# Kernel optimization log

Hardware: AMD Instinct MI355X
Metric: run time of the kernel (lower is better)

The kernel has to match this reference:

```python
import jax, jax.numpy as jnp
from jax import lax
import numpy as np

T, N, C, D, K = 256, 4096, 12, 256, 12


def setup_inputs() -> dict:
    key = jax.random.key(0)
    ks = jax.random.split(key, 11)
    g = lambda k, shape: (jax.random.normal(k, shape, jnp.float32) * 0.05)
    return {
        "x": jax.random.normal(ks[0], (T, N, C), jnp.float32),
        "enc_Wx": g(ks[1], (D, C)),
        "enc_bx": g(ks[2], (D,)),
        "enc_Wh": g(ks[3], (D, D)),
        "enc_Wy": g(ks[4], (K, D)),
        "enc_by": g(ks[5], (K,)),
        "dec_Wx": g(ks[6], (D, C)),
        "dec_bx": g(ks[7], (D,)),
        "dec_Wh": g(ks[8], (D, D)),
        "dec_Wy": g(ks[9], (K, D)),
        "dec_by": g(ks[10], (K,)),
    }


def reference(x, enc_Wx, enc_bx, enc_Wh, enc_Wy, enc_by,
              dec_Wx, dec_bx, dec_Wh, dec_Wy, dec_by):
    # x: (T, N, C)
    Tn, Nn, Cn = x.shape
    Dn = enc_Wh.shape[0]

    # ---- encoder Elman RNN: h_t = relu(x2h(x_t) + h2h(h_{t-1})) ----
    # Precompute input projection for all timesteps (batched GEMM),
    # leaving only the D x D recurrence inside the scan.
    x_proj = jnp.einsum('tnc,dc->tnd', x, enc_Wx) + enc_bx  # (T, N, D)

    def enc_step(h, xp):
        h = jax.nn.relu(xp + h @ enc_Wh.T)
        return h, None

    h0 = jnp.zeros((Nn, Dn), x.dtype)
    h_last, _ = lax.scan(enc_step, h0, x_proj)  # (N, D) == enc_h[-1]
    # (encoder h2y output is computed in the original but discarded)

    # ---- decoder: greedy feedback loop, T steps ----
    sos0 = jnp.zeros((Nn, Cn), x.dtype).at[:, -2].set(1.0)

    def dec_step(carry, _):
        h, sos = carry
        h = jax.nn.relu(sos @ dec_Wx.T + dec_bx + h @ dec_Wh.T)  # (N, D)
        y = h @ dec_Wy.T + dec_by                                # (N, K)
        sos = jax.nn.one_hot(jnp.argmax(y, axis=-1), y.shape[-1],
                             dtype=x.dtype)                      # (N, C)
        return (h, sos), y

    _, ys = lax.scan(dec_step, (h_last, sos0), None, length=Tn)
    return ys  # (T, N, K)
```

## Files before the change

### kernel.cpp

```cpp
#include <hip/hip_runtime.h>
#include <cstdint>
#include <cstddef>

#define TT 256
#define NN 4096
#define CC 12
#define DD 256
#define KD 12
#define NB 16
#define NTH 512
#define HS 264
#define XS 40
#define YS 20

typedef _Float16 half8 __attribute__((ext_vector_type(8)));
typedef float f32x4 __attribute__((ext_vector_type(4)));
#define MFMA __builtin_amdgcn_mfma_f32_16x16x32_f16

struct FalseC { static constexpr bool value = false; };
struct TrueC  { static constexpr bool value = true;  };

struct alignas(16) SM {
  _Float16 hhi[2][NB][HS];
  _Float16 hlo[2][NB][HS];
  _Float16 xhi[4][NB][XS];
  _Float16 xlo[4][NB][XS];
  float    part2[2][8][NB][YS];
};

__device__ __forceinline__ void split8(const float* w, half8& hi, half8& lo) {
  #pragma unroll
  for (int j = 0; j < 8; ++j) {
    _Float16 h = (_Float16)w[j];
    hi[j] = h;
    lo[j] = (_Float16)(w[j] - (float)h);
  }
}

__device__ __forceinline__ unsigned pack2(_Float16 a, _Float16 b) {
  union { _Float16 h[2]; unsigned u; } x;
  x.h[0] = a; x.h[1] = b;
  return x.u;
}

__device__ __forceinline__ void BAR() {
  asm volatile("s_waitcnt lgkmcnt(0)" ::: "memory");
  __builtin_amdgcn_s_barrier();
  __builtin_amdgcn_sched_barrier(0);
}

__global__ __launch_bounds__(NTH, 2)
void seq2seq_kernel(const float* __restrict__ x,
                    const float* __restrict__ enc_Wx,
                    const float* __restrict__ enc_bx,
                    const float* __restrict__ enc_Wh,
                    const float* __restrict__ dec_Wx,
                    const float* __restrict__ dec_bx,
                    const float* __restrict__ dec_Wh,
                    const float* __restrict__ dec_Wy,
                    const float* __restrict__ dec_by,
                    float* __restrict__ out)
{
  __shared__ SM sm;
  const int tid  = (int)threadIdx.x;
  const int wid  = tid >> 6;
  const int lane = tid & 63;
  const int l15  = lane & 15;
  const int quad = lane >> 4;
  const int n0   = (int)blockIdx.x * NB;

  half8 Whi[2][8], Wlo[2][8];
  half8 Xhi[2], Xlo[2];
  float bxr[2];
  float pfA0 = 0.f, pfA1 = 0.f, pfA2 = 0.f;
  float pfB0 = 0.f, pfB1 = 0.f, pfB2 = 0.f;

  if (wid == 1) {
    const float* xg = x + ((size_t)1 * NN + n0) * CC;
    pfB0 = xg[lane]; pfB1 = xg[lane + 64]; pfB2 = xg[lane + 128];
  }

  auto loadWh = [&](const float* __restrict__ W) {
    #pragma unroll
    for (int tt = 0; tt < 2; ++tt) {
      const int n = wid * 32 + 2 * l15 + tt;
      #pragma unroll
      for (int c = 0; c < 8; ++c) {
        float w[8];
        const float* p = W + (size_t)n * DD + c * 32 + quad * 8;
        *(float4*)&w[0] = *(const float4*)p;
        *(float4*)&w[4] = *(const float4*)(p + 4);
        split8(w, Whi[tt][c], Wlo[tt][c]);
      }
    }
  };
  auto loadWx = [&](const float* __restrict__ Wx) {
    #pragma unroll
    for (int tt = 0; tt < 2; ++tt) {
      const int n = wid * 32 + 2 * l15 + tt;
      float w[8];
      #pragma unroll
      for (int j = 0; j < 8; ++j) {
        const int k = quad * 8 + j;
        w[j] = (k < CC) ? Wx[(size_t)n * CC + k] : 0.f;
      }
      split8(w, Xhi[tt], Xlo[tt]);
    }
  };
  auto loadBx = [&](const float* __restrict__ bx) {
    #pragma unroll
    for (int tt = 0; tt < 2; ++tt) bxr[tt] = bx[wid * 32 + 2 * l15 + tt];
  };

  {
    unsigned* z;
    z = (unsigned*)&sm.hhi[0][0][0];
    for (int i = tid; i < NB * HS / 2; i += NTH) z[i] = 0u;
    z = (unsigned*)&sm.hlo[0][0][0];
    for (int i = tid; i < NB * HS / 2; i += NTH) z[i] = 0u;
    z = (unsigned*)&sm.xhi[0][0][0];
    for (int i = tid; i < 4 * NB * XS / 2; i += NTH) z[i] = 0u;
    z = (unsigned*)&sm.xlo[0][0][0];
    for (int i = tid; i < 4 * NB * XS / 2; i += NTH) z[i] = 0u;
  }
  loadWh(enc_Wh);
  loadWx(enc_Wx);
  loadBx(enc_bx);
  BAR();
  if (tid < NB * CC) {
    const float v = x[(size_t)n0 * CC + tid];
    const _Float16 h = (_Float16)v;
    sm.xhi[0][tid / CC][tid % CC] = h;
    sm.xlo[0][tid / CC][tid % CC] = (_Float16)(v - (float)h);
  }
  BAR();

  auto encStep = [&](int t, auto IAc) {
    constexpr bool IA = decltype(IAc)::value;
    if (wid == 1) {
      const int tp = (t + 2 < TT) ? (t + 2) : (TT - 1);
      const float* xg = x + ((size_t)tp * NN + n0) * CC;
      if constexpr (IA) { pfA0 = xg[lane]; pfA1 = xg[lane + 64]; pfA2 = xg[lane + 128]; }
      else              { pfB0 = xg[lane]; pfB1 = xg[lane + 64]; pfB2 = xg[lane + 128]; }
    }
    const int rb = t & 1, wb = rb ^ 1, xs = t & 3;
    f32x4 aA0 = {0.f,0.f,0.f,0.f}, aA1 = {0.f,0.f,0.f,0.f};
    f32x4 aB0 = {0.f,0.f,0.f,0.f}, aB1 = {0.f,0.f,0.f,0.f};
    const half8 xh = *(const half8*)&sm.xhi[xs][l15][quad * 8];
    const half8 xl = *(const half8*)&sm.xlo[xs][l15][quad * 8];
    aA0 = MFMA(xh, Xhi[0], aA0, 0, 0, 0);
    aA1 = MFMA(xh, Xhi[1], aA1, 0, 0, 0);
    aB0 = MFMA(xl, Xhi[0], aB0, 0, 0, 0);
    aB1 = MFMA(xl, Xhi[1], aB1, 0, 0, 0);
    aB0 = MFMA(xh, Xlo[0], aB0, 0, 0, 0);
    aB1 = MFMA(xh, Xlo[1], aB1, 0, 0, 0);
    const _Float16* hh = &sm.hhi[rb][l15][0];
    const _Float16* hl = &sm.hlo[rb][l15][0];
    #pragma unroll
    for (int c = 0; c < 8; ++c) {
      const half8 ahi = *(const half8*)(hh + c * 32 + quad * 8);
      const half8 alo = *(const half8*)(hl + c * 32 + quad * 8);
      aA0 = MFMA(ahi, Whi[0][c], aA0, 0, 0, 0);
      aA1 = MFMA(ahi, Whi[1][c], aA1, 0, 0, 0);
      aB0 = MFMA(alo, Whi[0][c], aB0, 0, 0, 0);
      aB1 = MFMA(alo, Whi[1][c], aB1, 0, 0, 0);
      aA0 = MFMA(ahi, Wlo[0][c], aA0, 0, 0, 0);
      aA1 = MFMA(ahi, Wlo[1][c], aA1, 0, 0, 0);
    }
    const int colh = wid * 32 + 2 * l15;
    #pragma unroll
    for (int r = 0; r < 4; ++r) {
      const int m = quad * 4 + r;
      const float v0 = fmaxf(aA0[r] + aB0[r] + bxr[0], 0.f);
      const float v1 = fmaxf(aA1[r] + aB1[r] + bxr[1], 0.f);
      const _Float16 h0 = (_Float16)v0, h1 = (_Float16)v1;
      *(unsigned*)&sm.hhi[wb][m][colh] = pack2(h0, h1);
      *(unsigned*)&sm.hlo[wb][m][colh] =
          pack2((_Float16)(v0 - (float)h0), (_Float16)(v1 - (float)h1));
    }
    if (wid == 1) {
      const int xw = (t + 1) & 3;
      float w0, w1, w2;
      if constexpr (IA) { w0 = pfB0; w1 = pfB1; w2 = pfB2; }
      else              { w0 = pfA0; w1 = pfA1; w2 = pfA2; }
      #pragma unroll
      for (int j = 0; j < 3; ++j) {
        const int i = lane + 64 * j;
        const float vv = (j == 0) ? w0 : (j == 1) ? w1 : w2;
        const _Float16 hx = (_Float16)vv;
        sm.xhi[xw][i / CC][i % CC] = hx;
        sm.xlo[xw][i / CC][i % CC] = (_Float16)(vv - (float)hx);
      }
    }
    BAR();
  };

  for (int t = 0; t < TT; t += 2) {
    encStep(t, TrueC{});
    encStep(t + 1, FalseC{});
  }

  loadWh(dec_Wh);
  loadWx(dec_Wx);
  loadBx(dec_bx);
  float by4[4];
  #pragma unroll
  for (int j = 0; j < 4; ++j) {
    const int o = quad * 4 + j;
    by4[j] = (o < KD) ? dec_by[o] : 0.f;
  }
  half8 wyh, wyl;
  {
    float w[8];
    if (l15 < KD) {
      const float* p = dec_Wy + (size_t)l15 * DD + wid * 32 + quad * 8;
      *(float4*)&w[0] = *(const float4*)p;
      *(float4*)&w[4] = *(const float4*)(p + 4);
    } else {
      #pragma unroll
      for (int j = 0; j < 8; ++j) w[j] = 0.f;
    }
    split8(w, wyh, wyl);
  }
  half8 aX;
  #pragma unroll
  for (int j = 0; j < 8; ++j)
    aX[j] = (_Float16)((quad * 8 + j == CC - 2) ? 1.f : 0.f);
  BAR();

  for (int t = 0; t < TT; ++t) {
    const int rb = t & 1, wb = rb ^ 1, pb = t & 1;
    f32x4 aA0 = {0.f,0.f,0.f,0.f}, aA1 = {0.f,0.f,0.f,0.f};
    f32x4 aB0 = {0.f,0.f,0.f,0.f}, aB1 = {0.f,0.f,0.f,0.f};
    aA0 = MFMA(aX, Xhi[0], aA0, 0, 0, 0);
    aA1 = MFMA(aX, Xhi[1], aA1, 0, 0, 0);
    aB0 = MFMA(aX, Xlo[0], aB0, 0, 0, 0);
    aB1 = MFMA(aX, Xlo[1], aB1, 0, 0, 0);
    const _Float16* hh = &sm.hhi[rb][l15][0];
    const _Float16* hl = &sm.hlo[rb][l15][0];
    #pragma unroll
    for (int c = 0; c < 8; ++c) {
      const half8 ahi = *(const half8*)(hh + c * 32 + quad * 8);
      const half8 alo = *(const half8*)(hl + c * 32 + quad * 8);
      aA0 = MFMA(ahi, Whi[0][c], aA0, 0, 0, 0);
      aA1 = MFMA(ahi, Whi[1][c], aA1, 0, 0, 0);
      aB0 = MFMA(alo, Whi[0][c], aB0, 0, 0, 0);
      aB1 = MFMA(alo, Whi[1][c], aB1, 0, 0, 0);
      aA0 = MFMA(ahi, Wlo[0][c], aA0, 0, 0, 0);
      aA1 = MFMA(ahi, Wlo[1][c], aA1, 0, 0, 0);
    }
    const int colh = wid * 32 + 2 * l15;
    #pragma unroll
    for (int r = 0; r < 4; ++r) {
      const int m = quad * 4 + r;
      const float v0 = fmaxf(aA0[r] + aB0[r] + bxr[0], 0.f);
      const float v1 = fmaxf(aA1[r] + aB1[r] + bxr[1], 0.f);
      const _Float16 h0 = (_Float16)v0, h1 = (_Float16)v1;
      *(unsigned*)&sm.hhi[wb][m][colh] = pack2(h0, h1);
      *(unsigned*)&sm.hlo[wb][m][colh] =
          pack2((_Float16)(v0 - (float)h0), (_Float16)(v1 - (float)h1));
    }
    asm volatile("s_waitcnt lgkmcnt(0)" ::: "memory");
    const half8 yh8 = *(const half8*)&sm.hhi[wb][l15][wid * 32 + quad * 8];
    const half8 yl8 = *(const half8*)&sm.hlo[wb][l15][wid * 32 + quad * 8];
    f32x4 yp = {0.f,0.f,0.f,0.f};
    yp = MFMA(yh8, wyh, yp, 0, 0, 0);
    yp = MFMA(yl8, wyh, yp, 0, 0, 0);
    yp = MFMA(yh8, wyl, yp, 0, 0, 0);
    #pragma unroll
    for (int r = 0; r < 4; ++r)
      sm.part2[pb][wid][quad * 4 + r][l15] = yp[r];
    BAR();
    f32x4 ys = *(const f32x4*)&sm.part2[pb][0][l15][quad * 4];
    #pragma unroll
    for (int w = 1; w < 8; ++w)
      ys += *(const f32x4*)&sm.part2[pb][w][l15][quad * 4];
    float yv[4];
    #pragma unroll
    for (int j = 0; j < 4; ++j) yv[j] = ys[j] + by4[j];
    if (wid == 0 && quad < 3) {
      float4 st; st.x = yv[0]; st.y = yv[1]; st.z = yv[2]; st.w = yv[3];
      *(float4*)&out[((size_t)t * NN + n0 + l15) * KD + quad * 4] = st;
    }
    float v = -1e30f; int io = 0;
    #pragma unroll
    for (int j = 0; j < 4; ++j) {
      const int o = quad * 4 + j;
      const float cv = (o < KD) ? yv[j] : -1e30f;
      const bool take = cv > v;
      io = take ? o : io;
      v  = take ? cv : v;
    }
    #pragma unroll
    for (int d = 16; d < 64; d <<= 1) {
      const float ov = __shfl_xor(v, d);
      const int   oi = __shfl_xor(io, d);
      const bool take = (ov > v) || (ov == v && oi < io);
      v  = take ? ov : v;
      io = take ? oi : io;
    }
    #pragma unroll
    for (int j = 0; j < 8; ++j)
      aX[j] = (_Float16)((quad * 8 + j == io) ? 1.f : 0.f);
  }
}

extern "C" void kernel_launch(void* const* d_in, const int* in_sizes, int n_in,
                              void* d_out, int out_size, void* d_ws, size_t ws_size,
                              hipStream_t stream) {
  (void)in_sizes; (void)n_in; (void)d_ws; (void)ws_size; (void)out_size;
  const float* x      = (const float*)d_in[0];
  const float* enc_Wx = (const float*)d_in[1];
  const float* enc_bx = (const float*)d_in[2];
  const float* enc_Wh = (const float*)d_in[3];
  const float* dec_Wx = (const float*)d_in[6];
  const float* dec_bx = (const float*)d_in[7];
  const float* dec_Wh = (const float*)d_in[8];
  const float* dec_Wy = (const float*)d_in[9];
  const float* dec_by = (const float*)d_in[10];
  float* outp = (float*)d_out;

  seq2seq_kernel<<<NN / NB, NTH, 0, stream>>>(
      x, enc_Wx, enc_bx, enc_Wh, dec_Wx, dec_bx, dec_Wh, dec_Wy, dec_by, outp);
}
```

Measured before the change: 820.5 us.

## Software-pipeline encoder input projection one step ahead and use packed fp16 conversion

The encoder now computes the input-projection MFMAs for step t+1 after the recurrent MFMAs of step t, keeping them in a second set of accumulators. This moves the x-projection and its LDS reads off the critical path that follows each barrier. The x prefetch distance grows by one step and two x slots are preloaded at start. Hidden-state hi/lo splitting now uses the packed round-toward-zero conversion (cvt_pkrtz) instead of separate scalar conversions, which changes rounding of the hi part, and the extra accumulators raise register pressure.

New measurement: 798.0 us. 2.7% less time.

```diff
diff --git a/kernel.cpp b/kernel.cpp
--- a/kernel.cpp
+++ b/kernel.cpp
@@ -14,6 +14,7 @@
 #define YS 20
 
 typedef _Float16 half8 __attribute__((ext_vector_type(8)));
+typedef __fp16 fp16x2 __attribute__((ext_vector_type(2)));
 typedef float f32x4 __attribute__((ext_vector_type(4)));
 #define MFMA __builtin_amdgcn_mfma_f32_16x16x32_f16
 
@@ -37,10 +38,13 @@
   }
 }
 
-__device__ __forceinline__ unsigned pack2(_Float16 a, _Float16 b) {
-  union { _Float16 h[2]; unsigned u; } x;
-  x.h[0] = a; x.h[1] = b;
-  return x.u;
+__device__ __forceinline__ void packpair(float v0, float v1,
+                                         unsigned& hw, unsigned& lw) {
+  union { fp16x2 v; unsigned u; } a, b;
+  a.v = __builtin_amdgcn_cvt_pkrtz(v0, v1);
+  const float r0 = (float)a.v[0], r1 = (float)a.v[1];
+  b.v = __builtin_amdgcn_cvt_pkrtz(v0 - r0, v1 - r1);
+  hw = a.u; lw = b.u;
 }
 
 __device__ __forceinline__ void BAR() {
@@ -74,11 +78,7 @@
   float bxr[2];
   float pfA0 = 0.f, pfA1 = 0.f, pfA2 = 0.f;
   float pfB0 = 0.f, pfB1 = 0.f, pfB2 = 0.f;
-
-  if (wid == 1) {
-    const float* xg = x + ((size_t)1 * NN + n0) * CC;
-    pfB0 = xg[lane]; pfB1 = xg[lane + 64]; pfB2 = xg[lane + 128];
-  }
+  f32x4 accP[4], accQ[4];
 
   auto loadWh = [&](const float* __restrict__ W) {
     #pragma unroll
@@ -126,67 +126,80 @@
   loadWh(enc_Wh);
   loadWx(enc_Wx);
   loadBx(enc_bx);
+  if (wid == 1) {
+    const float* xg = x + ((size_t)2 * NN + n0) * CC;
+    pfB0 = xg[lane]; pfB1 = xg[lane + 64]; pfB2 = xg[lane + 128];
+  }
   BAR();
-  if (tid < NB * CC) {
-    const float v = x[(size_t)n0 * CC + tid];
-    const _Float16 h = (_Float16)v;
-    sm.xhi[0][tid / CC][tid % CC] = h;
-    sm.xlo[0][tid / CC][tid % CC] = (_Float16)(v - (float)h);
+  #pragma unroll
+  for (int s = 0; s < 2; ++s) {
+    if (tid < NB * CC) {
+      const float v = x[((size_t)s * NN + n0) * CC + tid];
+      const _Float16 h = (_Float16)v;
+      sm.xhi[s][tid / CC][tid % CC] = h;
+      sm.xlo[s][tid / CC][tid % CC] = (_Float16)(v - (float)h);
+    }
   }
   BAR();
-
-  auto encStep = [&](int t, auto IAc) {
-    constexpr bool IA = decltype(IAc)::value;
-    if (wid == 1) {
-      const int tp = (t + 2 < TT) ? (t + 2) : (TT - 1);
-      const float* xg = x + ((size_t)tp * NN + n0) * CC;
-      if constexpr (IA) { pfA0 = xg[lane]; pfA1 = xg[lane + 64]; pfA2 = xg[lane + 128]; }
-      else              { pfB0 = xg[lane]; pfB1 = xg[lane + 64]; pfB2 = xg[lane + 128]; }
-    }
-    const int rb = t & 1, wb = rb ^ 1, xs = t & 3;
-    f32x4 aA0 = {0.f,0.f,0.f,0.f}, aA1 = {0.f,0.f,0.f,0.f};
-    f32x4 aB0 = {0.f,0.f,0.f,0.f}, aB1 = {0.f,0.f,0.f,0.f};
-    const half8 xh = *(const half8*)&sm.xhi[xs][l15][quad * 8];
-    const half8 xl = *(const half8*)&sm.xlo[xs][l15][quad * 8];
-    aA0 = MFMA(xh, Xhi[0], aA0, 0, 0, 0);
-    aA1 = MFMA(xh, Xhi[1], aA1, 0, 0, 0);
-    aB0 = MFMA(xl, Xhi[0], aB0, 0, 0, 0);
-    aB1 = MFMA(xl, Xhi[1], aB1, 0, 0, 0);
-    aB0 = MFMA(xh, Xlo[0], aB0, 0, 0, 0);
-    aB1 = MFMA(xh, Xlo[1], aB1, 0, 0, 0);
+  #pragma unroll
+  for (int i = 0; i < 4; ++i) accP[i] = (f32x4){0.f, 0.f, 0.f, 0.f};
+  {
+    const half8 xh = *(const half8*)&sm.xhi[0][l15][quad * 8];
+    const half8 xl = *(const half8*)&sm.xlo[0][l15][quad * 8];
+    accP[0] = MFMA(xh, Xhi[0], accP[0], 0, 0, 0);
+    accP[1] = MFMA(xh, Xhi[1], accP[1], 0, 0, 0);
+    accP[2] = MFMA(xl, Xhi[0], accP[2], 0, 0, 0);
+    accP[3] = MFMA(xl, Xhi[1], accP[3], 0, 0, 0);
+    accP[2] = MFMA(xh, Xlo[0], accP[2], 0, 0, 0);
+    accP[3] = MFMA(xh, Xlo[1], accP[3], 0, 0, 0);
+  }
+
+  auto encCore = [&](int t, f32x4 (&cur)[4], f32x4 (&nxt)[4],
+                     float pw0, float pw1, float pw2) {
+    const int rb = t & 1, wb = rb ^ 1;
     const _Float16* hh = &sm.hhi[rb][l15][0];
     const _Float16* hl = &sm.hlo[rb][l15][0];
     #pragma unroll
     for (int c = 0; c < 8; ++c) {
       const half8 ahi = *(const half8*)(hh + c * 32 + quad * 8);
       const half8 alo = *(const half8*)(hl + c * 32 + quad * 8);
-      aA0 = MFMA(ahi, Whi[0][c], aA0, 0, 0, 0);
-      aA1 = MFMA(ahi, Whi[1][c], aA1, 0, 0, 0);
-      aB0 = MFMA(alo, Whi[0][c], aB0, 0, 0, 0);
-      aB1 = MFMA(alo, Whi[1][c], aB1, 0, 0, 0);
-      aA0 = MFMA(ahi, Wlo[0][c], aA0, 0, 0, 0);
-      aA1 = MFMA(ahi, Wlo[1][c], aA1, 0, 0, 0);
+      cur[0] = MFMA(ahi, Whi[0][c], cur[0], 0, 0, 0);
+      cur[1] = MFMA(ahi, Whi[1][c], cur[1], 0, 0, 0);
+      cur[2] = MFMA(alo, Whi[0][c], cur[2], 0, 0, 0);
+      cur[3] = MFMA(alo, Whi[1][c], cur[3], 0, 0, 0);
+      cur[0] = MFMA(ahi, Wlo[0][c], cur[0], 0, 0, 0);
+      cur[1] = MFMA(ahi, Wlo[1][c], cur[1], 0, 0, 0);
+    }
+    #pragma unroll
+    for (int i = 0; i < 4; ++i) nxt[i] = (f32x4){0.f, 0.f, 0.f, 0.f};
+    if (t + 1 < TT) {
+      const int xs = (t + 1) & 3;
+      const half8 xh = *(const half8*)&sm.xhi[xs][l15][quad * 8];
+      const half8 xl = *(const half8*)&sm.xlo[xs][l15][quad * 8];
+      nxt[0] = MFMA(xh, Xhi[0], nxt[0], 0, 0, 0);
+      nxt[1] = MFMA(xh, Xhi[1], nxt[1], 0, 0, 0);
+      nxt[2] = MFMA(xl, Xhi[0], nxt[2], 0, 0, 0);
+      nxt[3] = MFMA(xl, Xhi[1], nxt[3], 0, 0, 0);
+      nxt[2] = MFMA(xh, Xlo[0], nxt[2], 0, 0, 0);
+      nxt[3] = MFMA(xh, Xlo[1], nxt[3], 0, 0, 0);
     }
     const int colh = wid * 32 + 2 * l15;
     #pragma unroll
     for (int r = 0; r < 4; ++r) {
       const int m = quad * 4 + r;
-      const float v0 = fmaxf(aA0[r] + aB0[r] + bxr[0], 0.f);
-      const float v1 = fmaxf(aA1[r] + aB1[r] + bxr[1], 0.f);
-      const _Float16 h0 = (_Float16)v0, h1 = (_Float16)v1;
-      *(unsigned*)&sm.hhi[wb][m][colh] = pack2(h0, h1);
-      *(unsigned*)&sm.hlo[wb][m][colh] =
-          pack2((_Float16)(v0 - (float)h0), (_Float16)(v1 - (float)h1));
+      const float v0 = fmaxf(cur[0][r] + cur[2][r] + bxr[0], 0.f);
+      const float v1 = fmaxf(cur[1][r] + cur[3][r] + bxr[1], 0.f);
+      unsigned hw, lw;
+      packpair(v0, v1, hw, lw);
+      *(unsigned*)&sm.hhi[wb][m][colh] = hw;
+      *(unsigned*)&sm.hlo[wb][m][colh] = lw;
     }
     if (wid == 1) {
-      const int xw = (t + 1) & 3;
-      float w0, w1, w2;
-      if constexpr (IA) { w0 = pfB0; w1 = pfB1; w2 = pfB2; }
-      else              { w0 = pfA0; w1 = pfA1; w2 = pfA2; }
+      const int xw = (t + 2) & 3;
       #pragma unroll
       for (int j = 0; j < 3; ++j) {
         const int i = lane + 64 * j;
-        const float vv = (j == 0) ? w0 : (j == 1) ? w1 : w2;
+        const float vv = (j == 0) ? pw0 : (j == 1) ? pw1 : pw2;
         const _Float16 hx = (_Float16)vv;
         sm.xhi[xw][i / CC][i % CC] = hx;
         sm.xlo[xw][i / CC][i % CC] = (_Float16)(vv - (float)hx);
@@ -195,9 +208,21 @@
     BAR();
   };
 
+  auto encBody = [&](int t, auto IAc) {
+    constexpr bool IA = decltype(IAc)::value;
+    if (wid == 1) {
+      const int tp = (t + 3 < TT) ? (t + 3) : (TT - 1);
+      const float* xg = x + ((size_t)tp * NN + n0) * CC;
+      if constexpr (IA) { pfA0 = xg[lane]; pfA1 = xg[lane + 64]; pfA2 = xg[lane + 128]; }
+      else              { pfB0 = xg[lane]; pfB1 = xg[lane + 64]; pfB2 = xg[lane + 128]; }
+    }
+    if constexpr (IA) encCore(t, accP, accQ, pfB0, pfB1, pfB2);
+    else              encCore(t, accQ, accP, pfA0, pfA1, pfA2);
+  };
+
   for (int t = 0; t < TT; t += 2) {
-    encStep(t, TrueC{});
-    encStep(t + 1, FalseC{});
+    encBody(t, TrueC{});
+    encBody(t + 1, FalseC{});
   }
 
   loadWh(dec_Wh);
@@ -255,10 +280,10 @@
       const int m = quad * 4 + r;
       const float v0 = fmaxf(aA0[r] + aB0[r] + bxr[0], 0.f);
       const float v1 = fmaxf(aA1[r] + aB1[r] + bxr[1], 0.f);
-      const _Float16 h0 = (_Float16)v0, h1 = (_Float16)v1;
-      *(unsigned*)&sm.hhi[wb][m][colh] = pack2(h0, h1);
-      *(unsigned*)&sm.hlo[wb][m][colh] =
-          pack2((_Float16)(v0 - (float)h0), (_Float16)(v1 - (float)h1));
+      unsigned hw, lw;
+      packpair(v0, v1, hw, lw);
+      *(unsigned*)&sm.hhi[wb][m][colh] = hw;
+      *(unsigned*)&sm.hlo[wb][m][colh] = lw;
     }
     asm volatile("s_waitcnt lgkmcnt(0)" ::: "memory");
     const half8 yh8 = *(const half8*)&sm.hhi[wb][l15][wid * 32 + quad * 8];
```
